# Kernel tuning notes

Hardware: AMD Instinct MI355X
Metric: run time of the kernel (lower is better)

The kernel has to match this reference:

```python
import jax, jax.numpy as jnp
import numpy as np

B, N, D_IN, D_MEM, LAYERS = 8, 2048, 128, 128, 3


def setup_inputs() -> dict:
    key = jax.random.key(0)
    k1, k2, k3, k4 = jax.random.split(key, 4)
    inputs = jax.random.normal(k1, (B, N, D_IN), dtype=jnp.float32)
    # attention-derived adjacency: nonnegative weights
    out_adj = jax.random.uniform(k2, (B, N, N), dtype=jnp.float32)
    # per-layer Linear weights (all layers 128->128 here, stacked) with
    # torch nn.Linear-style init scale 1/sqrt(fan_in)
    scale = 1.0 / np.sqrt(D_IN)
    W = jax.random.uniform(k3, (LAYERS, D_IN, D_MEM), minval=-scale, maxval=scale, dtype=jnp.float32)
    b = jax.random.uniform(k4, (LAYERS, D_MEM), minval=-scale, maxval=scale, dtype=jnp.float32)
    return {"inputs": inputs, "out_adj": out_adj, "W": W, "b": b}


def reference(inputs, out_adj, W, b):
    # GCN.forward (eval mode; dropout = identity)
    adj = out_adj  # [B, N, N]
    denom = jnp.sum(adj, axis=2, keepdims=True) + 1.0  # [B, N, 1]
    outputs = inputs  # [B, N, D]
    for l in range(W.shape[0]):
        Ax = jnp.einsum('bij,bjd->bid', adj, outputs)      # aggregate
        AxW = Ax @ W[l] + b[l]                             # per-layer linear
        outputs = jax.nn.relu(AxW / denom)                 # normalize + activate
    return outputs
```

## Files before the change

### kernel.cpp

```cpp
#include <hip/hip_runtime.h>

#define NN 2048
#define DD 128

typedef _Float16 f16x8 __attribute__((ext_vector_type(8)));
typedef float f32x4 __attribute__((ext_vector_type(4)));


__global__ __launch_bounds__(256) void prep_kernel(
    const float* __restrict__ W, _Float16* __restrict__ Wt) {
  int idx = blockIdx.x * 256 + threadIdx.x;
  int l = idx >> 14, r = idx & 16383, d = r >> 7, k = r & 127;
  Wt[idx] = (_Float16)W[l * 16384 + k * 128 + d];
}

__global__ __launch_bounds__(256) void prepAll_kernel(
    const float* __restrict__ adj, _Float16* __restrict__ adjH,
    float* __restrict__ rdg, const float* __restrict__ X,
    _Float16* __restrict__ Xt) {
  __shared__ float rs[16][4];
  const int bx = blockIdx.x, tid = threadIdx.x;
  const int lane = tid & 63, wave = tid >> 6;
  const int quad = lane >> 4, l15 = lane & 15;

  if (bx < 1024) {
    const int it = bx & 127, batch = bx >> 7;
    const float* Ap = adj + ((size_t)(batch * NN) + it * 16 + l15) * NN + quad * 8;
    _Float16* Hp = adjH + (size_t)batch * NN * NN + ((size_t)it * 64) * 512 + lane * 8;
    float s = 0.f;
#pragma unroll
    for (int j = 0; j < 16; ++j) {
      const int ct = wave + 4 * j;
      float4 a0 = *(const float4*)(Ap + ct * 32);
      float4 a1 = *(const float4*)(Ap + ct * 32 + 4);
      s += ((a0.x + a0.y) + (a0.z + a0.w)) + ((a1.x + a1.y) + (a1.z + a1.w));
      f16x8 h = {(_Float16)a0.x, (_Float16)a0.y, (_Float16)a0.z, (_Float16)a0.w,
                 (_Float16)a1.x, (_Float16)a1.y, (_Float16)a1.z, (_Float16)a1.w};
      *(f16x8*)(Hp + (size_t)ct * 512) = h;
    }
    s += __shfl_xor(s, 16);
    s += __shfl_xor(s, 32);
    if (lane < 16) rs[lane][wave] = s;
    __syncthreads();
    if (tid < 16) {
      float t = rs[tid][0] + rs[tid][1] + rs[tid][2] + rs[tid][3];
      rdg[batch * NN + it * 16 + tid] = 1.0f / (t + 1.0f);
    }
  } else if (bx < 1536) {
    const int vbx = bx - 1024;
    const int batch = vbx & 7, nt = vbx >> 3;
    const size_t batA = (size_t)batch * (128 * NN);
#pragma unroll
    for (int dtl = 0; dtl < 2; ++dtl) {
      const int dt = wave * 2 + dtl;
      const float* Xp = X + ((size_t)(batch * NN) + nt * 32 + quad * 8) * DD + dt * 16 + l15;
      f16x8 v;
#pragma unroll
      for (int e = 0; e < 8; ++e) v[e] = (_Float16)Xp[(size_t)e * DD];
      *(f16x8*)(Xt + batA + ((size_t)(dt * 64 + nt)) * 512 + lane * 8) = v;
    }
  }
}

__device__ __forceinline__ void epiGemm(const float (*Xs)[132],
    const _Float16* __restrict__ Wf, int d0, int quad, int l15,
    f32x4 (&o)[2][2]) {
#pragma unroll
  for (int kk = 0; kk < 128; kk += 32) {
    f16x8 a0 = *(const f16x8*)(Wf + (d0 + l15) * DD + kk + quad * 8);
    f16x8 a1 = *(const f16x8*)(Wf + (d0 + 16 + l15) * DD + kk + quad * 8);
#pragma unroll
    for (int fi = 0; fi < 2; ++fi) {
      const float* xp = &Xs[fi * 16 + l15][kk + quad * 8];
      f16x8 b = {(_Float16)xp[0], (_Float16)xp[1], (_Float16)xp[2], (_Float16)xp[3],
                 (_Float16)xp[4], (_Float16)xp[5], (_Float16)xp[6], (_Float16)xp[7]};
      o[0][fi] = __builtin_amdgcn_mfma_f32_16x16x32_f16(a0, b, o[0][fi], 0, 0, 0);
      o[1][fi] = __builtin_amdgcn_mfma_f32_16x16x32_f16(a1, b, o[1][fi], 0, 0, 0);
    }
  }
}

#define PD 8

template<int MODE>
__global__ __launch_bounds__(256) void aggP_kernel(
    const _Float16* __restrict__ adjH, const float* __restrict__ rdg,
    const _Float16* __restrict__ At, const float* __restrict__ bias,
    const _Float16* __restrict__ WA, const _Float16* __restrict__ WB,
    _Float16* __restrict__ Yout, float* __restrict__ out) {
  __shared__ float Xs[32][132];
  __shared__ float bsh[128];
  __shared__ float rdsh[32];

  const int tid = threadIdx.x, bx = blockIdx.x;
  const int batch = bx & 7, iblk = bx >> 3, i0 = iblk * 32;
  const int lane = tid & 63, wave = tid >> 6;
  const int quad = lane >> 4, l15 = lane & 15, d0 = wave * 32;

  const size_t batA = (size_t)batch * (128 * NN);
  const size_t batB = (size_t)batch * ((size_t)NN * NN);
  const int it0 = iblk * 2;
  const _Float16* Ap0 = At + batA + ((size_t)(2 * wave) * 64) * 512 + lane * 8;
  const _Float16* Ap1 = At + batA + ((size_t)(2 * wave + 1) * 64) * 512 + lane * 8;
  const _Float16* Bp0 = adjH + batB + ((size_t)it0 * 64) * 512 + lane * 8;
  const _Float16* Bp1 = adjH + batB + ((size_t)(it0 + 1) * 64) * 512 + lane * 8;

  if (tid < 128) bsh[tid] = bias[tid];
  if (tid < 32) rdsh[tid] = rdg[batch * NN + i0 + tid];

  f32x4 acc[2][2] = {};
  f16x8 qa0[PD], qa1[PD], qb0[PD], qb1[PD];

#define PF(j)                                              \
  { const int s_ = (j) & (PD - 1);                         \
    qa0[s_] = *(const f16x8*)(Ap0 + (size_t)(j) * 512);    \
    qa1[s_] = *(const f16x8*)(Ap1 + (size_t)(j) * 512);    \
    qb0[s_] = *(const f16x8*)(Bp0 + (size_t)(j) * 512);    \
    qb1[s_] = *(const f16x8*)(Bp1 + (size_t)(j) * 512); }
#define MM(j)                                                                                   \
  { const int s_ = (j) & (PD - 1);                                                              \
    acc[0][0] = __builtin_amdgcn_mfma_f32_16x16x32_f16(qa0[s_], qb0[s_], acc[0][0], 0, 0, 0);   \
    acc[0][1] = __builtin_amdgcn_mfma_f32_16x16x32_f16(qa0[s_], qb1[s_], acc[0][1], 0, 0, 0);   \
    acc[1][0] = __builtin_amdgcn_mfma_f32_16x16x32_f16(qa1[s_], qb0[s_], acc[1][0], 0, 0, 0);   \
    acc[1][1] = __builtin_amdgcn_mfma_f32_16x16x32_f16(qa1[s_], qb1[s_], acc[1][1], 0, 0, 0); }

#pragma unroll
  for (int j = 0; j < PD; ++j) PF(j)
#pragma unroll
  for (int ct = 0; ct < 64; ++ct) {
    MM(ct)
    if (ct + PD < 64) PF(ct + PD)
  }
#undef PF
#undef MM

  __syncthreads();
  const float rv0 = rdsh[l15], rv1 = rdsh[16 + l15];
  f32x4 accY[2][2];

  if (MODE == 0) {
#pragma unroll
    for (int df = 0; df < 2; ++df)
#pragma unroll
      for (int fi = 0; fi < 2; ++fi)
#pragma unroll
        for (int r = 0; r < 4; ++r)
          Xs[fi * 16 + l15][d0 + df * 16 + quad * 4 + r] = acc[df][fi][r];
    __syncthreads();
    f32x4 acc2[2][2] = {};
    epiGemm(Xs, WA, d0, quad, l15, acc2);
    __syncthreads();
#pragma unroll
    for (int df = 0; df < 2; ++df)
#pragma unroll
      for (int fi = 0; fi < 2; ++fi)
#pragma unroll
        for (int r = 0; r < 4; ++r) {
          int d = d0 + df * 16 + quad * 4 + r;
          float rv = fi ? rv1 : rv0;
          Xs[fi * 16 + l15][d] = fmaxf((acc2[df][fi][r] + bsh[d]) * rv, 0.f);
        }
    __syncthreads();
    f32x4 acc3[2][2] = {};
    epiGemm(Xs, WB, d0, quad, l15, acc3);
#pragma unroll
    for (int df = 0; df < 2; ++df)
#pragma unroll
      for (int fi = 0; fi < 2; ++fi) accY[df][fi] = acc3[df][fi];
  } else {
#pragma unroll
    for (int df = 0; df < 2; ++df)
#pragma unroll
      for (int fi = 0; fi < 2; ++fi)
#pragma unroll
        for (int r = 0; r < 4; ++r) {
          int d = d0 + df * 16 + quad * 4 + r;
          float rv = fi ? rv1 : rv0;
          Xs[fi * 16 + l15][d] = fmaxf((acc[df][fi][r] + bsh[d]) * rv, 0.f);
        }
    __syncthreads();
    if (MODE == 2) {
      float* outB = out + (size_t)(batch * NN + i0) * DD;
#pragma unroll
      for (int u = 0; u < 4; ++u) {
        int c = tid + 256 * u;
        int i = c >> 5, f4 = (c & 31) * 4;
        *(float4*)(outB + (size_t)i * DD + f4) = *(const float4*)&Xs[i][f4];
      }
      return;
    }
    f32x4 acc2[2][2] = {};
    epiGemm(Xs, WA, d0, quad, l15, acc2);
#pragma unroll
    for (int df = 0; df < 2; ++df)
#pragma unroll
      for (int fi = 0; fi < 2; ++fi) accY[df][fi] = acc2[df][fi];
  }

  __syncthreads();
  _Float16* Yst = (_Float16*)Xs;
#pragma unroll
  for (int df = 0; df < 2; ++df)
#pragma unroll
    for (int fi = 0; fi < 2; ++fi)
#pragma unroll
      for (int r = 0; r < 4; ++r)
        Yst[(d0 + df * 16 + quad * 4 + r) * 40 + fi * 16 + l15] =
            (_Float16)accY[df][fi][r];
  __syncthreads();
  const int nt = i0 >> 5;
  _Float16* Yb = Yout + batA;
#pragma unroll
  for (int dtl = 0; dtl < 2; ++dtl) {
    const int dt = 2 * wave + dtl;
    f16x8 v = *(const f16x8*)(&Yst[(dt * 16 + l15) * 40 + quad * 8]);
    *(f16x8*)(Yb + ((size_t)(dt * 64 + nt)) * 512 + lane * 8) = v;
  }
}

__global__ __launch_bounds__(256) void gemmY_kernel(
    const float* __restrict__ X, const _Float16* __restrict__ Wt,
    _Float16* __restrict__ Yt) {
  const int bx = blockIdx.x;
  const int batch = bx & 7, n0 = (bx >> 3) * 32;
  const int tid = threadIdx.x, lane = tid & 63, wave = tid >> 6;
  const int quad = lane >> 4, l15 = lane & 15, d0 = wave * 32;
  const float* Xb = X + (size_t)(batch * NN + n0) * DD;
  f32x4 acc[2][2] = {};
#pragma unroll
  for (int kk = 0; kk < 128; kk += 32) {
    f16x8 a0 = *(const f16x8*)(Wt + (d0 + l15) * DD + kk + quad * 8);
    f16x8 a1 = *(const f16x8*)(Wt + (d0 + 16 + l15) * DD + kk + quad * 8);
#pragma unroll
    for (int fi = 0; fi < 2; ++fi) {
      const float* xp = Xb + (size_t)(fi * 16 + l15) * DD + kk + quad * 8;
      float4 x0 = *(const float4*)xp;
      float4 x1 = *(const float4*)(xp + 4);
      f16x8 b = {(_Float16)x0.x, (_Float16)x0.y, (_Float16)x0.z, (_Float16)x0.w,
                 (_Float16)x1.x, (_Float16)x1.y, (_Float16)x1.z, (_Float16)x1.w};
      acc[0][fi] = __builtin_amdgcn_mfma_f32_16x16x32_f16(a0, b, acc[0][fi], 0, 0, 0);
      acc[1][fi] = __builtin_amdgcn_mfma_f32_16x16x32_f16(a1, b, acc[1][fi], 0, 0, 0);
    }
  }
  _Float16* YtB = Yt + (size_t)batch * DD * NN;
#pragma unroll
  for (int df = 0; df < 2; ++df)
#pragma unroll
    for (int fi = 0; fi < 2; ++fi)
#pragma unroll
      for (int r = 0; r < 4; ++r)
        YtB[(size_t)(d0 + df * 16 + quad * 4 + r) * NN + n0 + fi * 16 + l15] =
            (_Float16)acc[df][fi][r];
}

template<bool LAST>
__global__ __launch_bounds__(256) void agg_kernel(
    const float* __restrict__ adj, const _Float16* __restrict__ Yt,
    const float* __restrict__ bias, const _Float16* __restrict__ Wn,
    _Float16* __restrict__ Ytn, float* __restrict__ out) {
  __shared__ _Float16 Bsl[2][32 * 64];
  __shared__ float Xs[32][132];
  __shared__ float bsh[128];
  __shared__ float rd[32];

  const int tid = threadIdx.x, bx = blockIdx.x;
  const int batch = bx & 7, i0 = (bx >> 3) * 32;
  const int lane = tid & 63, wave = tid >> 6;
  const int quad = lane >> 4, l15 = lane & 15, d0 = wave * 32;
  const int ai = tid >> 3, ac = tid & 7;
  const int sc = ac ^ (ai & 7);

  const float* adjR = adj + (size_t)(batch * NN + i0 + ai) * NN + ac * 8;
  const _Float16* YtB = Yt + (size_t)batch * DD * NN;
  const _Float16* Ya0 = YtB + (size_t)(d0 + l15) * NN;
  const _Float16* Ya1 = YtB + (size_t)(d0 + 16 + l15) * NN;

  if (tid < 128) bsh[tid] = bias[tid];

  f32x4 acc[2][2] = {};
  float rowsum = 0.f;

  float4 av0 = *(const float4*)(adjR);
  float4 av1 = *(const float4*)(adjR + 4);
  f16x8 a[2][2];
#pragma unroll
  for (int k2 = 0; k2 < 2; ++k2) {
    a[k2][0] = *(const f16x8*)(Ya0 + k2 * 32 + quad * 8);
    a[k2][1] = *(const f16x8*)(Ya1 + k2 * 32 + quad * 8);
  }

  for (int ko = 0; ko < 32; ++ko) {
    rowsum += ((av0.x + av0.y) + (av0.z + av0.w)) + ((av1.x + av1.y) + (av1.z + av1.w));
    f16x8 h = {(_Float16)av0.x, (_Float16)av0.y, (_Float16)av0.z, (_Float16)av0.w,
               (_Float16)av1.x, (_Float16)av1.y, (_Float16)av1.z, (_Float16)av1.w};
    *(f16x8*)(&Bsl[ko & 1][ai * 64 + sc * 8]) = h;
    f16x8 an[2][2];
    if (ko < 31) {
      const int kb = (ko + 1) * 64;
      av0 = *(const float4*)(adjR + kb);
      av1 = *(const float4*)(adjR + kb + 4);
#pragma unroll
      for (int k2 = 0; k2 < 2; ++k2) {
        an[k2][0] = *(const f16x8*)(Ya0 + kb + k2 * 32 + quad * 8);
        an[k2][1] = *(const f16x8*)(Ya1 + kb + k2 * 32 + quad * 8);
      }
    }
    __syncthreads();
    const _Float16* B = Bsl[ko & 1];
#pragma unroll
    for (int k2 = 0; k2 < 2; ++k2)
#pragma unroll
      for (int fi = 0; fi < 2; ++fi) {
        const int row = fi * 16 + l15;
        const int ch = (k2 * 4 + quad) ^ (row & 7);
        f16x8 b = *(const f16x8*)(&B[row * 64 + ch * 8]);
        acc[0][fi] = __builtin_amdgcn_mfma_f32_16x16x32_f16(a[k2][0], b, acc[0][fi], 0, 0, 0);
        acc[1][fi] = __builtin_amdgcn_mfma_f32_16x16x32_f16(a[k2][1], b, acc[1][fi], 0, 0, 0);
      }
#pragma unroll
    for (int k2 = 0; k2 < 2; ++k2) { a[k2][0] = an[k2][0]; a[k2][1] = an[k2][1]; }
  }

  rowsum += __shfl_xor(rowsum, 1);
  rowsum += __shfl_xor(rowsum, 2);
  rowsum += __shfl_xor(rowsum, 4);
  if (ac == 0) rd[ai] = 1.0f / (rowsum + 1.0f);
  __syncthreads();

#pragma unroll
  for (int df = 0; df < 2; ++df)
#pragma unroll
    for (int fi = 0; fi < 2; ++fi)
#pragma unroll
      for (int r = 0; r < 4; ++r) {
        int d = d0 + df * 16 + quad * 4 + r;
        int i = fi * 16 + l15;
        Xs[i][d] = fmaxf((acc[df][fi][r] + bsh[d]) * rd[i], 0.f);
      }
  __syncthreads();

  if (LAST) {
    float* outB = out + (size_t)(batch * NN + i0) * DD;
#pragma unroll
    for (int u = 0; u < 4; ++u) {
      int c = tid + 256 * u;
      int i = c >> 5, f4 = (c & 31) * 4;
      *(float4*)(outB + (size_t)i * DD + f4) = *(const float4*)&Xs[i][f4];
    }
  } else {
    f32x4 acc2[2][2] = {};
    epiGemm(Xs, Wn, d0, quad, l15, acc2);
    _Float16* YnB = Ytn + (size_t)batch * DD * NN;
#pragma unroll
    for (int df = 0; df < 2; ++df)
#pragma unroll
      for (int fi = 0; fi < 2; ++fi)
#pragma unroll
        for (int r = 0; r < 4; ++r)
          YnB[(size_t)(d0 + df * 16 + quad * 4 + r) * NN + i0 + fi * 16 + l15] =
              (_Float16)acc2[df][fi][r];
  }
}

extern "C" void kernel_launch(void* const* d_in, const int* in_sizes, int n_in,
                              void* d_out, int out_size, void* d_ws, size_t ws_size,
                              hipStream_t stream) {
  const float* x0   = (const float*)d_in[0];
  const float* adj  = (const float*)d_in[1];
  const float* W    = (const float*)d_in[2];
  const float* bias = (const float*)d_in[3];
  float* out = (float*)d_out;

  _Float16* Wt   = (_Float16*)d_ws;
  float*    rdg  = (float*)((char*)d_ws + (1u << 17));
  _Float16* Xt   = (_Float16*)((char*)d_ws + (1u << 20));
  _Float16* Y1t  = (_Float16*)((char*)d_ws + (5u << 20));
  _Float16* Y2t  = (_Float16*)((char*)d_ws + (9u << 20));
  _Float16* adjH = (_Float16*)((char*)d_ws + (16u << 20));

  const bool big = ws_size >= (81ull << 20);

  dim3 blk(256);
  prep_kernel<<<192, blk, 0, stream>>>(W, Wt);
  if (big) {
    prepAll_kernel<<<1536, blk, 0, stream>>>(adj, adjH, rdg, x0, Xt);
    aggP_kernel<0><<<512, blk, 0, stream>>>(adjH, rdg, Xt, bias, Wt, Wt + 16384, Y1t, nullptr);
    aggP_kernel<1><<<512, blk, 0, stream>>>(adjH, rdg, Y1t, bias + 128, Wt + 32768, nullptr, Y2t, nullptr);
    aggP_kernel<2><<<512, blk, 0, stream>>>(adjH, rdg, Y2t, bias + 256, nullptr, nullptr, nullptr, out);
  } else {
    _Float16* YtA  = Xt;
    _Float16* YtB_ = (_Float16*)d_out;
    gemmY_kernel<<<512, blk, 0, stream>>>(x0, Wt, YtA);
    agg_kernel<false><<<512, blk, 0, stream>>>(adj, YtA,  bias,       Wt + 16384, YtB_, nullptr);
    agg_kernel<false><<<512, blk, 0, stream>>>(adj, YtB_, bias + 128, Wt + 32768, YtA,  nullptr);
    agg_kernel<true ><<<512, blk, 0, stream>>>(adj, YtA,  bias + 256, nullptr,    nullptr, out);
  }
}
```

Measured before the change: 290.6 us.

## Fuse all GCN stages into one cooperative kernel with grid syncs

Replaces the five separate launches (weight prep, adjacency/X prep, three aggregation layers) with a single cooperative kernel of 512 blocks that uses grid-wide syncs between stages, aiming to remove launch gaps and tail effects between kernels. The aggregation prefetch depth is reduced from 8 to 4 stages to lower register pressure so two blocks fit per CU, which the cooperative launch needs for residency. The trade-off is grid.sync overhead and shallower load pipelining, with a fallback to the multi-kernel path if the cooperative launch fails.

```diff
diff --git a/kernel.cpp b/kernel.cpp
--- a/kernel.cpp
+++ b/kernel.cpp
@@ -1,4 +1,7 @@
 #include <hip/hip_runtime.h>
+#include <hip/hip_cooperative_groups.h>
+
+namespace cg = cooperative_groups;
 
 #define NN 2048
 #define DD 128
@@ -6,6 +9,232 @@
 typedef _Float16 f16x8 __attribute__((ext_vector_type(8)));
 typedef float f32x4 __attribute__((ext_vector_type(4)));
 
+
+__device__ __forceinline__ void epiGemm(const float (*Xs)[132],
+    const _Float16* __restrict__ Wf, int d0, int quad, int l15,
+    f32x4 (&o)[2][2]) {
+#pragma unroll
+  for (int kk = 0; kk < 128; kk += 32) {
+    f16x8 a0 = *(const f16x8*)(Wf + (d0 + l15) * DD + kk + quad * 8);
+    f16x8 a1 = *(const f16x8*)(Wf + (d0 + 16 + l15) * DD + kk + quad * 8);
+#pragma unroll
+    for (int fi = 0; fi < 2; ++fi) {
+      const float* xp = &Xs[fi * 16 + l15][kk + quad * 8];
+      f16x8 b = {(_Float16)xp[0], (_Float16)xp[1], (_Float16)xp[2], (_Float16)xp[3],
+                 (_Float16)xp[4], (_Float16)xp[5], (_Float16)xp[6], (_Float16)xp[7]};
+      o[0][fi] = __builtin_amdgcn_mfma_f32_16x16x32_f16(a0, b, o[0][fi], 0, 0, 0);
+      o[1][fi] = __builtin_amdgcn_mfma_f32_16x16x32_f16(a1, b, o[1][fi], 0, 0, 0);
+    }
+  }
+}
+
+__device__ __forceinline__ void aggMain(const _Float16* __restrict__ At,
+    const _Float16* __restrict__ adjHb, size_t batA, size_t batB,
+    int wave, int lane, int iblk, f32x4 (&acc)[2][2]) {
+  const int it0 = iblk * 2;
+  const _Float16* Ap0 = At + batA + ((size_t)(2 * wave) * 64) * 512 + lane * 8;
+  const _Float16* Ap1 = At + batA + ((size_t)(2 * wave + 1) * 64) * 512 + lane * 8;
+  const _Float16* Bp0 = adjHb + batB + ((size_t)it0 * 64) * 512 + lane * 8;
+  const _Float16* Bp1 = adjHb + batB + ((size_t)(it0 + 1) * 64) * 512 + lane * 8;
+  f16x8 qa0[4], qa1[4], qb0[4], qb1[4];
+#define PF(j)                                              \
+  { const int s_ = (j) & 3;                                \
+    qa0[s_] = *(const f16x8*)(Ap0 + (size_t)(j) * 512);    \
+    qa1[s_] = *(const f16x8*)(Ap1 + (size_t)(j) * 512);    \
+    qb0[s_] = *(const f16x8*)(Bp0 + (size_t)(j) * 512);    \
+    qb1[s_] = *(const f16x8*)(Bp1 + (size_t)(j) * 512); }
+#define MM(j)                                                                                   \
+  { const int s_ = (j) & 3;                                                                     \
+    acc[0][0] = __builtin_amdgcn_mfma_f32_16x16x32_f16(qa0[s_], qb0[s_], acc[0][0], 0, 0, 0);   \
+    acc[0][1] = __builtin_amdgcn_mfma_f32_16x16x32_f16(qa0[s_], qb1[s_], acc[0][1], 0, 0, 0);   \
+    acc[1][0] = __builtin_amdgcn_mfma_f32_16x16x32_f16(qa1[s_], qb0[s_], acc[1][0], 0, 0, 0);   \
+    acc[1][1] = __builtin_amdgcn_mfma_f32_16x16x32_f16(qa1[s_], qb1[s_], acc[1][1], 0, 0, 0); }
+  PF(0) PF(1) PF(2) PF(3)
+#pragma unroll
+  for (int ct = 0; ct < 64; ++ct) {
+    MM(ct)
+    if (ct + 4 < 64) PF(ct + 4)
+  }
+#undef PF
+#undef MM
+}
+
+__device__ __forceinline__ void fragStoreY(float (*Xs)[132],
+    const f32x4 (&accY)[2][2], _Float16* __restrict__ Yb, int i0,
+    int wave, int quad, int l15, int lane, int d0) {
+  __syncthreads();
+  _Float16* Yst = (_Float16*)Xs;
+#pragma unroll
+  for (int df = 0; df < 2; ++df)
+#pragma unroll
+    for (int fi = 0; fi < 2; ++fi)
+#pragma unroll
+      for (int r = 0; r < 4; ++r)
+        Yst[(d0 + df * 16 + quad * 4 + r) * 40 + fi * 16 + l15] =
+            (_Float16)accY[df][fi][r];
+  __syncthreads();
+  const int nt = i0 >> 5;
+#pragma unroll
+  for (int dtl = 0; dtl < 2; ++dtl) {
+    const int dt = 2 * wave + dtl;
+    f16x8 v = *(const f16x8*)(&Yst[(dt * 16 + l15) * 40 + quad * 8]);
+    *(f16x8*)(Yb + ((size_t)(dt * 64 + nt)) * 512 + lane * 8) = v;
+  }
+}
+
+__global__ __launch_bounds__(256, 2) void fused_kernel(
+    const float* __restrict__ adj, const float* __restrict__ X,
+    const float* __restrict__ W, const float* __restrict__ bias,
+    _Float16* __restrict__ adjH, float* __restrict__ rdg,
+    _Float16* __restrict__ Xt, _Float16* __restrict__ Y1t,
+    _Float16* __restrict__ Y2t, _Float16* __restrict__ Wt,
+    float* __restrict__ out) {
+  __shared__ float Xs[32][132];
+  __shared__ float bsh[384];
+  __shared__ float rdsh[32];
+  __shared__ float rs[16][4];
+
+  cg::grid_group grid = cg::this_grid();
+
+  const int tid = threadIdx.x, bx = blockIdx.x;
+  const int lane = tid & 63, wave = tid >> 6;
+  const int quad = lane >> 4, l15 = lane & 15, d0 = wave * 32;
+
+  bsh[tid] = bias[tid];
+  if (tid < 128) bsh[256 + tid] = bias[256 + tid];
+
+  if (bx < 192) {
+    int idx = bx * 256 + tid;
+    int l = idx >> 14, r = idx & 16383, d = r >> 7, k = r & 127;
+    Wt[idx] = (_Float16)W[l * 16384 + k * 128 + d];
+  }
+#pragma unroll
+  for (int u = 0; u < 2; ++u) {
+    const int unit = bx * 2 + u;
+    const int it = unit & 127, batch = unit >> 7;
+    const float* Ap = adj + ((size_t)(batch * NN) + it * 16 + l15) * NN + quad * 8;
+    _Float16* Hp = adjH + (size_t)batch * NN * NN + ((size_t)it * 64) * 512 + lane * 8;
+    float s = 0.f;
+#pragma unroll
+    for (int j = 0; j < 16; ++j) {
+      const int ct = wave + 4 * j;
+      float4 a0 = *(const float4*)(Ap + ct * 32);
+      float4 a1 = *(const float4*)(Ap + ct * 32 + 4);
+      s += ((a0.x + a0.y) + (a0.z + a0.w)) + ((a1.x + a1.y) + (a1.z + a1.w));
+      f16x8 h = {(_Float16)a0.x, (_Float16)a0.y, (_Float16)a0.z, (_Float16)a0.w,
+                 (_Float16)a1.x, (_Float16)a1.y, (_Float16)a1.z, (_Float16)a1.w};
+      *(f16x8*)(Hp + (size_t)ct * 512) = h;
+    }
+    s += __shfl_xor(s, 16);
+    s += __shfl_xor(s, 32);
+    if (lane < 16) rs[lane][wave] = s;
+    __syncthreads();
+    if (tid < 16) {
+      float t = rs[tid][0] + rs[tid][1] + rs[tid][2] + rs[tid][3];
+      rdg[batch * NN + it * 16 + tid] = 1.0f / (t + 1.0f);
+    }
+    __syncthreads();
+  }
+  {
+    const int batch = bx & 7, nt = bx >> 3;
+    const size_t batA = (size_t)batch * (128 * NN);
+#pragma unroll
+    for (int dtl = 0; dtl < 2; ++dtl) {
+      const int dt = wave * 2 + dtl;
+      const float* Xp = X + ((size_t)(batch * NN) + nt * 32 + quad * 8) * DD + dt * 16 + l15;
+      f16x8 v;
+#pragma unroll
+      for (int e = 0; e < 8; ++e) v[e] = (_Float16)Xp[(size_t)e * DD];
+      *(f16x8*)(Xt + batA + ((size_t)(dt * 64 + nt)) * 512 + lane * 8) = v;
+    }
+  }
+  grid.sync();
+
+  const int batch = bx & 7, iblk = bx >> 3, i0 = iblk * 32;
+  const size_t batA = (size_t)batch * (128 * NN);
+  const size_t batB = (size_t)batch * ((size_t)NN * NN);
+  if (tid < 32) rdsh[tid] = rdg[batch * NN + i0 + tid];
+
+  {
+    f32x4 acc[2][2] = {};
+    aggMain(Xt, adjH, batA, batB, wave, lane, iblk, acc);
+    __syncthreads();
+#pragma unroll
+    for (int df = 0; df < 2; ++df)
+#pragma unroll
+      for (int fi = 0; fi < 2; ++fi)
+#pragma unroll
+        for (int r = 0; r < 4; ++r)
+          Xs[fi * 16 + l15][d0 + df * 16 + quad * 4 + r] = acc[df][fi][r];
+    __syncthreads();
+    f32x4 acc2[2][2] = {};
+    epiGemm(Xs, Wt, d0, quad, l15, acc2);
+    __syncthreads();
+    const float rv0 = rdsh[l15], rv1 = rdsh[16 + l15];
+#pragma unroll
+    for (int df = 0; df < 2; ++df)
+#pragma unroll
+      for (int fi = 0; fi < 2; ++fi)
+#pragma unroll
+        for (int r = 0; r < 4; ++r) {
+          int d = d0 + df * 16 + quad * 4 + r;
+          float rv = fi ? rv1 : rv0;
+          Xs[fi * 16 + l15][d] = fmaxf((acc2[df][fi][r] + bsh[d]) * rv, 0.f);
+        }
+    __syncthreads();
+    f32x4 acc3[2][2] = {};
+    epiGemm(Xs, Wt + 16384, d0, quad, l15, acc3);
+    fragStoreY(Xs, acc3, Y1t + batA, i0, wave, quad, l15, lane, d0);
+  }
+  grid.sync();
+
+  {
+    f32x4 acc[2][2] = {};
+    aggMain(Y1t, adjH, batA, batB, wave, lane, iblk, acc);
+    __syncthreads();
+    const float rv0 = rdsh[l15], rv1 = rdsh[16 + l15];
+#pragma unroll
+    for (int df = 0; df < 2; ++df)
+#pragma unroll
+      for (int fi = 0; fi < 2; ++fi)
+#pragma unroll
+        for (int r = 0; r < 4; ++r) {
+          int d = d0 + df * 16 + quad * 4 + r;
+          float rv = fi ? rv1 : rv0;
+          Xs[fi * 16 + l15][d] = fmaxf((acc[df][fi][r] + bsh[128 + d]) * rv, 0.f);
+        }
+    __syncthreads();
+    f32x4 acc2[2][2] = {};
+    epiGemm(Xs, Wt + 32768, d0, quad, l15, acc2);
+    fragStoreY(Xs, acc2, Y2t + batA, i0, wave, quad, l15, lane, d0);
+  }
+  grid.sync();
+
+  {
+    f32x4 acc[2][2] = {};
+    aggMain(Y2t, adjH, batA, batB, wave, lane, iblk, acc);
+    __syncthreads();
+    const float rv0 = rdsh[l15], rv1 = rdsh[16 + l15];
+#pragma unroll
+    for (int df = 0; df < 2; ++df)
+#pragma unroll
+      for (int fi = 0; fi < 2; ++fi)
+#pragma unroll
+        for (int r = 0; r < 4; ++r) {
+          int d = d0 + df * 16 + quad * 4 + r;
+          float rv = fi ? rv1 : rv0;
+          Xs[fi * 16 + l15][d] = fmaxf((acc[df][fi][r] + bsh[256 + d]) * rv, 0.f);
+        }
+    __syncthreads();
+    float* outB = out + (size_t)(batch * NN + i0) * DD;
+#pragma unroll
+    for (int u = 0; u < 4; ++u) {
+      int c = tid + 256 * u;
+      int i = c >> 5, f4 = (c & 31) * 4;
+      *(float4*)(outB + (size_t)i * DD + f4) = *(const float4*)&Xs[i][f4];
+    }
+  }
+}
 
 __global__ __launch_bounds__(256) void prep_kernel(
     const float* __restrict__ W, _Float16* __restrict__ Wt) {
@@ -61,26 +290,6 @@
     }
   }
 }
-
-__device__ __forceinline__ void epiGemm(const float (*Xs)[132],
-    const _Float16* __restrict__ Wf, int d0, int quad, int l15,
-    f32x4 (&o)[2][2]) {
-#pragma unroll
-  for (int kk = 0; kk < 128; kk += 32) {
-    f16x8 a0 = *(const f16x8*)(Wf + (d0 + l15) * DD + kk + quad * 8);
-    f16x8 a1 = *(const f16x8*)(Wf + (d0 + 16 + l15) * DD + kk + quad * 8);
-#pragma unroll
-    for (int fi = 0; fi < 2; ++fi) {
-      const float* xp = &Xs[fi * 16 + l15][kk + quad * 8];
-      f16x8 b = {(_Float16)xp[0], (_Float16)xp[1], (_Float16)xp[2], (_Float16)xp[3],
-                 (_Float16)xp[4], (_Float16)xp[5], (_Float16)xp[6], (_Float16)xp[7]};
-      o[0][fi] = __builtin_amdgcn_mfma_f32_16x16x32_f16(a0, b, o[0][fi], 0, 0, 0);
-      o[1][fi] = __builtin_amdgcn_mfma_f32_16x16x32_f16(a1, b, o[1][fi], 0, 0, 0);
-    }
-  }
-}
-
-#define PD 8
 
 template<int MODE>
 __global__ __launch_bounds__(256) void aggP_kernel(
@@ -99,40 +308,12 @@
 
   const size_t batA = (size_t)batch * (128 * NN);
   const size_t batB = (size_t)batch * ((size_t)NN * NN);
-  const int it0 = iblk * 2;
-  const _Float16* Ap0 = At + batA + ((size_t)(2 * wave) * 64) * 512 + lane * 8;
-  const _Float16* Ap1 = At + batA + ((size_t)(2 * wave + 1) * 64) * 512 + lane * 8;
-  const _Float16* Bp0 = adjH + batB + ((size_t)it0 * 64) * 512 + lane * 8;
-  const _Float16* Bp1 = adjH + batB + ((size_t)(it0 + 1) * 64) * 512 + lane * 8;
 
   if (tid < 128) bsh[tid] = bias[tid];
   if (tid < 32) rdsh[tid] = rdg[batch * NN + i0 + tid];
 
   f32x4 acc[2][2] = {};
-  f16x8 qa0[PD], qa1[PD], qb0[PD], qb1[PD];
-
-#define PF(j)                                              \
-  { const int s_ = (j) & (PD - 1);                         \
-    qa0[s_] = *(const f16x8*)(Ap0 + (size_t)(j) * 512);    \
-    qa1[s_] = *(const f16x8*)(Ap1 + (size_t)(j) * 512);    \
-    qb0[s_] = *(const f16x8*)(Bp0 + (size_t)(j) * 512);    \
-    qb1[s_] = *(const f16x8*)(Bp1 + (size_t)(j) * 512); }
-#define MM(j)                                                                                   \
-  { const int s_ = (j) & (PD - 1);                                                              \
-    acc[0][0] = __builtin_amdgcn_mfma_f32_16x16x32_f16(qa0[s_], qb0[s_], acc[0][0], 0, 0, 0);   \
-    acc[0][1] = __builtin_amdgcn_mfma_f32_16x16x32_f16(qa0[s_], qb1[s_], acc[0][1], 0, 0, 0);   \
-    acc[1][0] = __builtin_amdgcn_mfma_f32_16x16x32_f16(qa1[s_], qb0[s_], acc[1][0], 0, 0, 0);   \
-    acc[1][1] = __builtin_amdgcn_mfma_f32_16x16x32_f16(qa1[s_], qb1[s_], acc[1][1], 0, 0, 0); }
-
-#pragma unroll
-  for (int j = 0; j < PD; ++j) PF(j)
-#pragma unroll
-  for (int ct = 0; ct < 64; ++ct) {
-    MM(ct)
-    if (ct + PD < 64) PF(ct + PD)
-  }
-#undef PF
-#undef MM
+  aggMain(At, adjH, batA, batB, wave, lane, iblk, acc);
 
   __syncthreads();
   const float rv0 = rdsh[l15], rv1 = rdsh[16 + l15];
@@ -197,25 +378,7 @@
       for (int fi = 0; fi < 2; ++fi) accY[df][fi] = acc2[df][fi];
   }
 
-  __syncthreads();
-  _Float16* Yst = (_Float16*)Xs;
-#pragma unroll
-  for (int df = 0; df < 2; ++df)
-#pragma unroll
-    for (int fi = 0; fi < 2; ++fi)
-#pragma unroll
-      for (int r = 0; r < 4; ++r)
-        Yst[(d0 + df * 16 + quad * 4 + r) * 40 + fi * 16 + l15] =
-            (_Float16)accY[df][fi][r];
-  __syncthreads();
-  const int nt = i0 >> 5;
-  _Float16* Yb = Yout + batA;
-#pragma unroll
-  for (int dtl = 0; dtl < 2; ++dtl) {
-    const int dt = 2 * wave + dtl;
-    f16x8 v = *(const f16x8*)(&Yst[(dt * 16 + l15) * 40 + quad * 8]);
-    *(f16x8*)(Yb + ((size_t)(dt * 64 + nt)) * 512 + lane * 8) = v;
-  }
+  fragStoreY(Xs, accY, Yout + batA, i0, wave, quad, l15, lane, d0);
 }
 
 __global__ __launch_bounds__(256) void gemmY_kernel(
@@ -379,10 +542,16 @@
   _Float16* adjH = (_Float16*)((char*)d_ws + (16u << 20));
 
   const bool big = ws_size >= (81ull << 20);
-
   dim3 blk(256);
-  prep_kernel<<<192, blk, 0, stream>>>(W, Wt);
+
   if (big) {
+    void* kargs[] = {(void*)&adj, (void*)&x0, (void*)&W, (void*)&bias,
+                     (void*)&adjH, (void*)&rdg, (void*)&Xt, (void*)&Y1t,
+                     (void*)&Y2t, (void*)&Wt, (void*)&out};
+    hipError_t e = hipLaunchCooperativeKernel((const void*)fused_kernel,
+        dim3(512), blk, kargs, 0, stream);
+    if (e == hipSuccess) return;
+    prep_kernel<<<192, blk, 0, stream>>>(W, Wt);
     prepAll_kernel<<<1536, blk, 0, stream>>>(adj, adjH, rdg, x0, Xt);
     aggP_kernel<0><<<512, blk, 0, stream>>>(adjH, rdg, Xt, bias, Wt, Wt + 16384, Y1t, nullptr);
     aggP_kernel<1><<<512, blk, 0, stream>>>(adjH, rdg, Y1t, bias + 128, Wt + 32768, nullptr, Y2t, nullptr);
@@ -390,6 +559,7 @@
   } else {
     _Float16* YtA  = Xt;
     _Float16* YtB_ = (_Float16*)d_out;
+    prep_kernel<<<192, blk, 0, stream>>>(W, Wt);
     gemmY_kernel<<<512, blk, 0, stream>>>(x0, Wt, YtA);
     agg_kernel<false><<<512, blk, 0, stream>>>(adj, YtA,  bias,       Wt + 16384, YtB_, nullptr);
     agg_kernel<false><<<512, blk, 0, stream>>>(adj, YtB_, bias + 128, Wt + 32768, YtA,  nullptr);
```

Result: slower. 543.4 us (+87.0%).

## Share adjacency tiles across waves via double-buffered LDS in aggregation kernel

Applied to the files above, without the earlier changes.

Before, every wave loaded the same two adjacency row-tiles straight from global memory into registers. Now the four waves split the adjacency load, with each wave fetching 4 of 16 fragments per chunk, stage it through a double-buffered shared-memory tile, and then all waves read it from LDS. This cuts redundant global or L2 traffic on the fp16 adjacency by about four times. The trade-off is a __syncthreads per chunk, extra LDS use (32KB) that may lower occupancy, and a shallower A prefetch (4 instead of 8).

```diff
diff --git a/kernel.cpp b/kernel.cpp
--- a/kernel.cpp
+++ b/kernel.cpp
@@ -80,14 +80,94 @@
   }
 }
 
-#define PD 8
+__device__ __forceinline__ void aggMainC(const _Float16* __restrict__ At,
+    const _Float16* __restrict__ adjHb, size_t batA, size_t batB,
+    int wave, int lane, int iblk, _Float16* __restrict__ Bs,
+    f32x4 (&acc)[2][2]) {
+  const int it0 = iblk * 2;
+  const _Float16* Ap0 = At + batA + ((size_t)(2 * wave) * 64) * 512 + lane * 8;
+  const _Float16* Ap1 = At + batA + ((size_t)(2 * wave + 1) * 64) * 512 + lane * 8;
+  const _Float16* Bq0 = adjHb + batB + ((size_t)it0 * 64) * 512 + lane * 8;
+  const _Float16* Bq1 = adjHb + batB + ((size_t)(it0 + 1) * 64) * 512 + lane * 8;
+
+  const int t0 = wave * 4;
+
+  f16x8 sreg[4];
+#pragma unroll
+  for (int j = 0; j < 4; ++j) {
+    const int t = t0 + j, cl = t >> 1, rt = t & 1;
+    sreg[j] = *(const f16x8*)((rt ? Bq1 : Bq0) + (size_t)cl * 512);
+  }
+  f16x8 qa0[4], qa1[4];
+#pragma unroll
+  for (int j = 0; j < 4; ++j) {
+    qa0[j] = *(const f16x8*)(Ap0 + (size_t)j * 512);
+    qa1[j] = *(const f16x8*)(Ap1 + (size_t)j * 512);
+  }
+
+#pragma unroll
+  for (int ch = 0; ch < 8; ++ch) {
+    _Float16* buf = Bs + (ch & 1) * (16 * 512);
+#pragma unroll
+    for (int j = 0; j < 4; ++j)
+      *(f16x8*)(buf + (t0 + j) * 512 + lane * 8) = sreg[j];
+    if (ch < 7) {
+#pragma unroll
+      for (int j = 0; j < 4; ++j) {
+        const int t = t0 + j, cl = t >> 1, rt = t & 1;
+        sreg[j] = *(const f16x8*)((rt ? Bq1 : Bq0) +
+                                  (size_t)((ch + 1) * 8 + cl) * 512);
+      }
+    }
+    __syncthreads();
+#pragma unroll
+    for (int c = 0; c < 8; ++c) {
+      const int ct = ch * 8 + c;
+      const int s = ct & 3;
+      f16x8 b0 = *(const f16x8*)(buf + (c * 2 + 0) * 512 + lane * 8);
+      f16x8 b1 = *(const f16x8*)(buf + (c * 2 + 1) * 512 + lane * 8);
+      acc[0][0] = __builtin_amdgcn_mfma_f32_16x16x32_f16(qa0[s], b0, acc[0][0], 0, 0, 0);
+      acc[0][1] = __builtin_amdgcn_mfma_f32_16x16x32_f16(qa0[s], b1, acc[0][1], 0, 0, 0);
+      acc[1][0] = __builtin_amdgcn_mfma_f32_16x16x32_f16(qa1[s], b0, acc[1][0], 0, 0, 0);
+      acc[1][1] = __builtin_amdgcn_mfma_f32_16x16x32_f16(qa1[s], b1, acc[1][1], 0, 0, 0);
+      if (ct + 4 < 64) {
+        qa0[s] = *(const f16x8*)(Ap0 + (size_t)(ct + 4) * 512);
+        qa1[s] = *(const f16x8*)(Ap1 + (size_t)(ct + 4) * 512);
+      }
+    }
+  }
+}
+
+__device__ __forceinline__ void fragStoreY(float (*Xs)[132],
+    const f32x4 (&accY)[2][2], _Float16* __restrict__ Yb, int i0,
+    int wave, int quad, int l15, int lane, int d0) {
+  __syncthreads();
+  _Float16* Yst = (_Float16*)Xs;
+#pragma unroll
+  for (int df = 0; df < 2; ++df)
+#pragma unroll
+    for (int fi = 0; fi < 2; ++fi)
+#pragma unroll
+      for (int r = 0; r < 4; ++r)
+        Yst[(d0 + df * 16 + quad * 4 + r) * 40 + fi * 16 + l15] =
+            (_Float16)accY[df][fi][r];
+  __syncthreads();
+  const int nt = i0 >> 5;
+#pragma unroll
+  for (int dtl = 0; dtl < 2; ++dtl) {
+    const int dt = 2 * wave + dtl;
+    f16x8 v = *(const f16x8*)(&Yst[(dt * 16 + l15) * 40 + quad * 8]);
+    *(f16x8*)(Yb + ((size_t)(dt * 64 + nt)) * 512 + lane * 8) = v;
+  }
+}
 
 template<int MODE>
-__global__ __launch_bounds__(256) void aggP_kernel(
+__global__ __launch_bounds__(256) void aggC_kernel(
     const _Float16* __restrict__ adjH, const float* __restrict__ rdg,
     const _Float16* __restrict__ At, const float* __restrict__ bias,
     const _Float16* __restrict__ WA, const _Float16* __restrict__ WB,
     _Float16* __restrict__ Yout, float* __restrict__ out) {
+  __shared__ _Float16 Bs[2][16 * 512];
   __shared__ float Xs[32][132];
   __shared__ float bsh[128];
   __shared__ float rdsh[32];
@@ -99,40 +179,12 @@
 
   const size_t batA = (size_t)batch * (128 * NN);
   const size_t batB = (size_t)batch * ((size_t)NN * NN);
-  const int it0 = iblk * 2;
-  const _Float16* Ap0 = At + batA + ((size_t)(2 * wave) * 64) * 512 + lane * 8;
-  const _Float16* Ap1 = At + batA + ((size_t)(2 * wave + 1) * 64) * 512 + lane * 8;
-  const _Float16* Bp0 = adjH + batB + ((size_t)it0 * 64) * 512 + lane * 8;
-  const _Float16* Bp1 = adjH + batB + ((size_t)(it0 + 1) * 64) * 512 + lane * 8;
 
   if (tid < 128) bsh[tid] = bias[tid];
   if (tid < 32) rdsh[tid] = rdg[batch * NN + i0 + tid];
 
   f32x4 acc[2][2] = {};
-  f16x8 qa0[PD], qa1[PD], qb0[PD], qb1[PD];
-
-#define PF(j)                                              \
-  { const int s_ = (j) & (PD - 1);                         \
-    qa0[s_] = *(const f16x8*)(Ap0 + (size_t)(j) * 512);    \
-    qa1[s_] = *(const f16x8*)(Ap1 + (size_t)(j) * 512);    \
-    qb0[s_] = *(const f16x8*)(Bp0 + (size_t)(j) * 512);    \
-    qb1[s_] = *(const f16x8*)(Bp1 + (size_t)(j) * 512); }
-#define MM(j)                                                                                   \
-  { const int s_ = (j) & (PD - 1);                                                              \
-    acc[0][0] = __builtin_amdgcn_mfma_f32_16x16x32_f16(qa0[s_], qb0[s_], acc[0][0], 0, 0, 0);   \
-    acc[0][1] = __builtin_amdgcn_mfma_f32_16x16x32_f16(qa0[s_], qb1[s_], acc[0][1], 0, 0, 0);   \
-    acc[1][0] = __builtin_amdgcn_mfma_f32_16x16x32_f16(qa1[s_], qb0[s_], acc[1][0], 0, 0, 0);   \
-    acc[1][1] = __builtin_amdgcn_mfma_f32_16x16x32_f16(qa1[s_], qb1[s_], acc[1][1], 0, 0, 0); }
-
-#pragma unroll
-  for (int j = 0; j < PD; ++j) PF(j)
-#pragma unroll
-  for (int ct = 0; ct < 64; ++ct) {
-    MM(ct)
-    if (ct + PD < 64) PF(ct + PD)
-  }
-#undef PF
-#undef MM
+  aggMainC(At, adjH, batA, batB, wave, lane, iblk, &Bs[0][0], acc);
 
   __syncthreads();
   const float rv0 = rdsh[l15], rv1 = rdsh[16 + l15];
@@ -197,25 +249,7 @@
       for (int fi = 0; fi < 2; ++fi) accY[df][fi] = acc2[df][fi];
   }
 
-  __syncthreads();
-  _Float16* Yst = (_Float16*)Xs;
-#pragma unroll
-  for (int df = 0; df < 2; ++df)
-#pragma unroll
-    for (int fi = 0; fi < 2; ++fi)
-#pragma unroll
-      for (int r = 0; r < 4; ++r)
-        Yst[(d0 + df * 16 + quad * 4 + r) * 40 + fi * 16 + l15] =
-            (_Float16)accY[df][fi][r];
-  __syncthreads();
-  const int nt = i0 >> 5;
-  _Float16* Yb = Yout + batA;
-#pragma unroll
-  for (int dtl = 0; dtl < 2; ++dtl) {
-    const int dt = 2 * wave + dtl;
-    f16x8 v = *(const f16x8*)(&Yst[(dt * 16 + l15) * 40 + quad * 8]);
-    *(f16x8*)(Yb + ((size_t)(dt * 64 + nt)) * 512 + lane * 8) = v;
-  }
+  fragStoreY(Xs, accY, Yout + batA, i0, wave, quad, l15, lane, d0);
 }
 
 __global__ __launch_bounds__(256) void gemmY_kernel(
@@ -379,14 +413,14 @@
   _Float16* adjH = (_Float16*)((char*)d_ws + (16u << 20));
 
   const bool big = ws_size >= (81ull << 20);
-
   dim3 blk(256);
+
   prep_kernel<<<192, blk, 0, stream>>>(W, Wt);
   if (big) {
     prepAll_kernel<<<1536, blk, 0, stream>>>(adj, adjH, rdg, x0, Xt);
-    aggP_kernel<0><<<512, blk, 0, stream>>>(adjH, rdg, Xt, bias, Wt, Wt + 16384, Y1t, nullptr);
-    aggP_kernel<1><<<512, blk, 0, stream>>>(adjH, rdg, Y1t, bias + 128, Wt + 32768, nullptr, Y2t, nullptr);
-    aggP_kernel<2><<<512, blk, 0, stream>>>(adjH, rdg, Y2t, bias + 256, nullptr, nullptr, nullptr, out);
+    aggC_kernel<0><<<512, blk, 0, stream>>>(adjH, rdg, Xt, bias, Wt, Wt + 16384, Y1t, nullptr);
+    aggC_kernel<1><<<512, blk, 0, stream>>>(adjH, rdg, Y1t, bias + 128, Wt + 32768, nullptr, Y2t, nullptr);
+    aggC_kernel<2><<<512, blk, 0, stream>>>(adjH, rdg, Y2t, bias + 256, nullptr, nullptr, nullptr, out);
   } else {
     _Float16* YtA  = Xt;
     _Float16* YtB_ = (_Float16*)d_out;
```

Result: faster. 270.4 us (-7.0%).
